# Kernel tuning notes

Measured on AMD Instinct MI355X. Metric: run time of the kernel, lower is better.

## Reference

```python
import jax, jax.numpy as jnp
import numpy as np
from jax import lax

K, INC, OUC = 6, 64, 32
H, W = 512, 512
WIN = 128  # min(128, min(H,W)) for training path
ITERATION = 2  # torch uses random.randint(1,3); fixed for determinism


def setup_inputs() -> dict:
    key = jax.random.key(0)
    ks = jax.random.split(key, 12)
    s = 0.05
    return {
        "x": jax.random.uniform(ks[0], (K, 3, H, W), jnp.float32),
        "pred_list": jax.random.uniform(ks[1], (K, 3, H, W), jnp.float32),
        "feat_list": jax.random.normal(ks[2], (K, INC, H, W), jnp.float32) * 0.1,
        "split_w": jax.random.normal(ks[3], (3 * OUC, INC, 3, 3), jnp.float32) * s,
        "split_b": jax.random.normal(ks[4], (3 * OUC,), jnp.float32) * s,
        "merge1_w": jax.random.normal(ks[5], (INC, 3 * OUC + 3, 3, 3), jnp.float32) * s,
        "merge1_b": jax.random.normal(ks[6], (INC,), jnp.float32) * s,
        "merge2_w": jax.random.normal(ks[7], (INC, INC, 3, 3), jnp.float32) * s,
        "merge2_b": jax.random.normal(ks[8], (INC,), jnp.float32) * s,
        "head_w": jax.random.normal(ks[9], (3, INC, 3, 3), jnp.float32) * s,
        "head_b": jax.random.normal(ks[10], (3,), jnp.float32) * s,
    }


def _conv(x, w, b, groups=1):
    y = lax.conv_general_dilated(
        x, w, (1, 1), ((1, 1), (1, 1)),
        dimension_numbers=("NCHW", "OIHW", "NCHW"), feature_group_count=groups)
    return y + b[None, :, None, None]


def _get_box(pred_list):
    # B_cat = mean of bg channel, T_cat = sum of fg channel; distance map [H,W]
    B_cat = pred_list[:, 2].mean(axis=0)
    T_cat = pred_list[:, 0].sum(axis=0)
    distance = jnp.abs(1.0 - T_cat - B_cat)
    # nearest-neighbor downsample by 0.1: out[i,j] = in[10*i, 10*j]
    hs, ws = H // 10, W // 10
    ds = distance[::10, ::10][:hs, :ws]
    # NMS keep[0] (training path uses boxes[0:1]) == global argmax of score
    idx = jnp.argmax(ds.reshape(-1))
    cx = (idx % ws) * 10
    cy = (idx // ws) * 10
    half = WIN // 2
    x1, y1 = cx - half, cy - half
    x2, y2 = cx + half, cy + half
    ox = (-jnp.minimum(x1, 0) + jnp.minimum(W - x1, 0)
          - jnp.minimum(x2, 0) + jnp.minimum(W - x2, 0))
    oy = (-jnp.minimum(y1, 0) + jnp.minimum(H - y1, 0)
          - jnp.minimum(y2, 0) + jnp.minimum(H - y2, 0))
    return (y1 + oy).astype(jnp.int32), (x1 + ox).astype(jnp.int32)


def reference(x, pred_list, feat_list, split_w, split_b,
              merge1_w, merge1_b, merge2_w, merge2_b, head_w, head_b):
    c = INC
    y1, x1 = _get_box(pred_list)  # box fixed across iterations (computed once)
    x_patch = lax.dynamic_slice(x, (0, 0, y1, x1), (K, 3, WIN, WIN))
    feat_patch = lax.dynamic_slice(feat_list, (0, 0, y1, x1), (K, INC, WIN, WIN))
    feat_tiled = jnp.tile(feat_patch, (1, 3, 1, 1))
    denom = max(K - 1, 1)

    pl = pred_list
    for _ in range(ITERATION):
        pred_patch = lax.dynamic_slice(pl, (0, 0, y1, x1), (K, 3, WIN, WIN))
        # cat([p0.repeat(c), p1.repeat(c), p2.repeat(c)]) == repeat each channel c times
        attention = jnp.repeat(pred_patch, c, axis=1)
        fs = _conv(feat_tiled * attention, split_w, split_b, groups=3)
        f0, f1, f2 = fs[:, :OUC], fs[:, OUC:2 * OUC], fs[:, 2 * OUC:]
        feat_t = f1.sum(0, keepdims=True) / denom - f0.sum(0, keepdims=True) + 2.0 * f0
        feat_r = f0.sum(0, keepdims=True) - f0 + f1
        feat_b = jnp.broadcast_to(f2.mean(0, keepdims=True), f2.shape)
        fcat = jnp.concatenate([feat_t, feat_r, feat_b, x_patch], axis=1)
        h1 = jax.nn.leaky_relu(_conv(fcat, merge1_w, merge1_b), 0.2)
        fm = _conv(h1, merge2_w, merge2_b)
        pr = _conv(fm, head_w, head_b)
        inner = (jnp.tanh(pr[:, :, 10:WIN - 10, 10:WIN - 10]) + 1.0) / 2.0
        pl = lax.dynamic_update_slice(pl, inner, (0, 0, y1 + 10, x1 + 10))
    return pl
```

## Files before the change

### kernel.cpp

```cpp
#include <hip/hip_runtime.h>
#include <math.h>

typedef __attribute__((ext_vector_type(8))) short short8_t;
typedef __attribute__((ext_vector_type(4))) float f32x4;

#define Hh 512
#define Ww 512
#define IMG (Hh * Ww)
#define WINP 128
#define PP (WINP * WINP)
#define QS 325

__device__ __forceinline__ unsigned short f2bf(float f) {
    unsigned int u = __builtin_bit_cast(unsigned int, f);
    u += 0x7fffu + ((u >> 16) & 1u);
    return (unsigned short)(u >> 16);
}
__device__ __forceinline__ float bf2f(unsigned short h) {
    unsigned int u = ((unsigned int)h) << 16;
    return __builtin_bit_cast(float, u);
}

__global__ void box_kernel(const float* __restrict__ pred, int* __restrict__ box) {
    int tid = threadIdx.x;
    float best = -1.0f; int bidx = 0x7fffffff;
    for (int cand = tid; cand < 51 * 51; cand += 256) {
        int i = cand / 51, j = cand % 51;
        int y = i * 10, x = j * 10;
        float T = 0.f, Bv = 0.f;
#pragma unroll
        for (int k = 0; k < 6; ++k) {
            T  += pred[((k * 3 + 0) * Hh + y) * Ww + x];
            Bv += pred[((k * 3 + 2) * Hh + y) * Ww + x];
        }
        float d = fabsf(1.0f - T - Bv / 6.0f);
        if (d > best || (d == best && cand < bidx)) { best = d; bidx = cand; }
    }
    __shared__ float sv[256];
    __shared__ int   si[256];
    sv[tid] = best; si[tid] = bidx;
    __syncthreads();
    for (int s = 128; s > 0; s >>= 1) {
        if (tid < s) {
            if (sv[tid + s] > sv[tid] || (sv[tid + s] == sv[tid] && si[tid + s] < si[tid])) {
                sv[tid] = sv[tid + s]; si[tid] = si[tid + s];
            }
        }
        __syncthreads();
    }
    if (tid == 0) {
        int idx = si[0];
        int cy = (idx / 51) * 10, cx = (idx % 51) * 10;
        int yy = cy - 64; yy = yy < 0 ? 0 : (yy > Hh - WINP ? Hh - WINP : yy);
        int xx = cx - 64; xx = xx < 0 ? 0 : (xx > Ww - WINP ? Ww - WINP : xx);
        box[0] = yy; box[1] = xx;
    }
}

__global__ void copy_kernel(const float4* __restrict__ src, float4* __restrict__ dst) {
    int i = blockIdx.x * 256 + threadIdx.x;
    dst[i] = src[i];
}

__global__ void prep_weights(const float* __restrict__ sw, const float* __restrict__ m1w,
                             const float* __restrict__ m2w, const float* __restrict__ hw,
                             unsigned short* __restrict__ WF)
{
    int idx = blockIdx.x * 256 + threadIdx.x;
    int j = idx & 7;
    int lane = (idx >> 3) & 63;
    int frag = idx >> 9;
    int n16 = lane & 15;
    int ko = (lane >> 4) * 8 + j;
    float v = 0.f;
    if (frag < 108) {
        int g = frag / 36; int r = frag % 36; int kc = r / 18; r %= 18; int tap = r / 2; int nf = r & 1;
        int oc = g * 32 + nf * 16 + n16; int ic = kc * 32 + ko;
        v = sw[(oc * 64 + ic) * 9 + tap];
    } else if (frag < 252) {
        int r = frag - 108; int half = r / 72; r %= 72; int kc = r / 18; r %= 18; int tap = r / 2; int nf = r & 1;
        int oc = half * 32 + nf * 16 + n16; int ic = kc * 32 + ko;
        if (ic < 99) v = m1w[(oc * 99 + ic) * 9 + tap];
    } else if (frag < 324) {
        int r = frag - 252; int half = r / 36; r %= 36; int kc = r / 18; r %= 18; int tap = r / 2; int nf = r & 1;
        int oc = half * 32 + nf * 16 + n16; int ic = kc * 32 + ko;
        v = m2w[(oc * 64 + ic) * 9 + tap];
    } else {
        int r = frag - 324; int kc = r / 9; int tap = r % 9;
        int ic = kc * 32 + ko;
        if (n16 < 3) v = hw[(n16 * 64 + ic) * 9 + tap];
    }
    WF[idx] = f2bf(v);
}

__global__ void prep_featcl(const float* __restrict__ feat, const int* __restrict__ box,
                            unsigned short* __restrict__ featcl)
{
    int row = blockIdx.x;
    int k = blockIdx.y;
    int t = threadIdx.x;
    int y1 = box[0], x1 = box[1];
    __shared__ unsigned short s[128 * 64];
    for (int i = 0; i < 32; ++i) {
        int idx = t + i * 256;
        int ic = idx >> 7, c = idx & 127;
        s[c * 64 + ic] = f2bf(feat[((size_t)(k * 64 + ic) * Hh + y1 + row) * Ww + x1 + c]);
    }
    __syncthreads();
    if (t < 128) {
        unsigned short* dst = &featcl[((size_t)k * 16384 + row * 128 + t) * 64];
        for (int i = 0; i < 8; ++i)
            *(short8_t*)&dst[i * 8] = *(short8_t*)&s[t * 64 + i * 8];
    }
}

__global__ __launch_bounds__(256) void split_mfma(
    const unsigned short* __restrict__ featcl, const float* __restrict__ pl,
    const unsigned short* __restrict__ WF, const float* __restrict__ sb,
    const int* __restrict__ box, unsigned short* __restrict__ fscl)
{
    const int tid = threadIdx.x;
    const int l = tid & 63, w = tid >> 6;
    const int T = blockIdx.x;
    const int k = blockIdx.y / 3, g = blockIdx.y % 3;
    const int ty0 = (T >> 3) * 16, tx0 = (T & 7) * 16;
    const int y1 = box[0], x1 = box[1];

    __shared__ __align__(16) unsigned short s_a[4 * QS * 8];
    __shared__ __align__(16) unsigned short s_b[9216];

    f32x4 acc[4][2];
#pragma unroll
    for (int mf = 0; mf < 4; ++mf)
#pragma unroll
        for (int nf = 0; nf < 2; ++nf) acc[mf][nf] = (f32x4){0.f, 0.f, 0.f, 0.f};

    const float* plg = pl + (size_t)(k * 3 + g) * IMG + (size_t)y1 * Ww + x1;
    const unsigned short* fck = featcl + (size_t)k * 16384 * 64;

    for (int kc = 0; kc < 2; ++kc) {
        __syncthreads();
#pragma unroll
        for (int i = 0; i < 6; ++i) {
            int s = tid + i * 256;
            if (s < 1296) {
                int pxs = s >> 2, q = s & 3;
                int r = pxs / 18, c = pxs - r * 18;
                int py = ty0 - 1 + r, px = tx0 - 1 + c;
                short8_t o;
                if (py >= 0 && py < WINP && px >= 0 && px < WINP) {
                    float pv = plg[py * Ww + px];
                    short8_t f = *(const short8_t*)&fck[(size_t)(py * WINP + px) * 64 + kc * 32 + q * 8];
#pragma unroll
                    for (int e = 0; e < 8; ++e) o[e] = (short)f2bf(bf2f((unsigned short)f[e]) * pv);
                } else {
#pragma unroll
                    for (int e = 0; e < 8; ++e) o[e] = 0;
                }
                *(short8_t*)&s_a[(q * QS + pxs) * 8] = o;
            }
        }
        {
            const unsigned short* src = WF + (size_t)((g * 2 + kc) * 18) * 512;
#pragma unroll
            for (int i = 0; i < 5; ++i) {
                int cch = tid + i * 256;
                if (cch < 1152)
                    *(short8_t*)&s_b[cch * 8] = *(const short8_t*)&src[cch * 8];
            }
        }
        __syncthreads();
#pragma unroll
        for (int tap = 0; tap < 9; ++tap) {
            int dy = tap / 3, dx = tap % 3;
            short8_t a[4];
#pragma unroll
            for (int mf = 0; mf < 4; ++mf)
                a[mf] = *(const short8_t*)&s_a[((l >> 4) * QS + (w * 4 + mf + dy) * 18 + (l & 15) + dx) * 8];
#pragma unroll
            for (int nf = 0; nf < 2; ++nf) {
                short8_t bfr = *(const short8_t*)&s_b[((tap * 2 + nf) * 64 + l) * 8];
#pragma unroll
                for (int mf = 0; mf < 4; ++mf)
                    acc[mf][nf] = __builtin_amdgcn_mfma_f32_16x16x32_bf16(a[mf], bfr, acc[mf][nf], 0, 0, 0);
            }
        }
    }
    __syncthreads();
    unsigned short* s_t = s_a;
#pragma unroll
    for (int nf = 0; nf < 2; ++nf) {
        float bias = sb[g * 32 + nf * 16 + (l & 15)];
        int slot = nf * 2 + ((l & 15) >> 3);
#pragma unroll
        for (int mf = 0; mf < 4; ++mf) {
            int row = w * 4 + mf;
#pragma unroll
            for (int r = 0; r < 4; ++r) {
                int col = (l >> 4) * 4 + r;
                s_t[(slot * 256 + row * 16 + col) * 8 + (l & 7)] = f2bf(acc[mf][nf][r] + bias);
            }
        }
    }
    __syncthreads();
    {
        int row = tid >> 4, col = tid & 15;
        size_t gpx = (size_t)(ty0 + row) * WINP + tx0 + col;
        unsigned short* dst = fscl + ((size_t)k * 16384 + gpx) * 96 + g * 32;
#pragma unroll
        for (int i = 0; i < 4; ++i)
            *(short8_t*)&dst[i * 8] = *(short8_t*)&s_t[(i * 256 + tid) * 8];
    }
}

__global__ void reduce_kernel(const unsigned short* __restrict__ fscl, float* __restrict__ Scl)
{
    int tg = blockIdx.x * 256 + threadIdx.x;
    int px = tg >> 2, q = tg & 3;
    float s0[8], s1[8], s2[8];
#pragma unroll
    for (int e = 0; e < 8; ++e) { s0[e] = 0.f; s1[e] = 0.f; s2[e] = 0.f; }
#pragma unroll
    for (int k = 0; k < 6; ++k) {
        const unsigned short* p = &fscl[((size_t)k * 16384 + px) * 96 + q * 8];
        short8_t a0 = *(const short8_t*)&p[0];
        short8_t a1 = *(const short8_t*)&p[32];
        short8_t a2 = *(const short8_t*)&p[64];
#pragma unroll
        for (int e = 0; e < 8; ++e) {
            s0[e] += bf2f((unsigned short)a0[e]);
            s1[e] += bf2f((unsigned short)a1[e]);
            s2[e] += bf2f((unsigned short)a2[e]);
        }
    }
    float* d = &Scl[(size_t)px * 96 + q * 8];
#pragma unroll
    for (int e = 0; e < 8; ++e) {
        d[e]      = s1[e] * 0.2f - s0[e];
        d[32 + e] = s0[e];
        d[64 + e] = s2[e] * (1.f / 6.f);
    }
}

__global__ __launch_bounds__(256) void merge1_mfma(
    const unsigned short* __restrict__ fscl, const float* __restrict__ Scl,
    const float* __restrict__ x, const unsigned short* __restrict__ WF,
    const float* __restrict__ m1b, const int* __restrict__ box,
    unsigned short* __restrict__ h1cl)
{
    const int tid = threadIdx.x;
    const int l = tid & 63, w = tid >> 6;
    const int T = blockIdx.x;
    const int k = blockIdx.y >> 1, half = blockIdx.y & 1;
    const int ty0 = (T >> 3) * 16, tx0 = (T & 7) * 16;
    const int y1 = box[0], x1 = box[1];

    __shared__ __align__(16) unsigned short s_a[4 * QS * 8];
    __shared__ __align__(16) unsigned short s_b[9216];

    f32x4 acc[4][2];
#pragma unroll
    for (int mf = 0; mf < 4; ++mf)
#pragma unroll
        for (int nf = 0; nf < 2; ++nf) acc[mf][nf] = (f32x4){0.f, 0.f, 0.f, 0.f};

    for (int kc = 0; kc < 4; ++kc) {
        __syncthreads();
#pragma unroll
        for (int i = 0; i < 6; ++i) {
            int s = tid + i * 256;
            if (s < 1296) {
                int pxs = s >> 2, q = s & 3;
                int r = pxs / 18, c = pxs - r * 18;
                int py = ty0 - 1 + r, px = tx0 - 1 + c;
                short8_t o;
#pragma unroll
                for (int e = 0; e < 8; ++e) o[e] = 0;
                if (py >= 0 && py < WINP && px >= 0 && px < WINP) {
                    size_t gpx = (size_t)py * WINP + px;
                    if (kc == 0) {
                        short8_t f0 = *(const short8_t*)&fscl[((size_t)k * 16384 + gpx) * 96 + q * 8];
                        const float* S = &Scl[gpx * 96 + q * 8];
#pragma unroll
                        for (int e = 0; e < 8; ++e)
                            o[e] = (short)f2bf(S[e] + 2.f * bf2f((unsigned short)f0[e]));
                    } else if (kc == 1) {
                        const unsigned short* fp = &fscl[((size_t)k * 16384 + gpx) * 96];
                        short8_t f0 = *(const short8_t*)&fp[q * 8];
                        short8_t f1 = *(const short8_t*)&fp[32 + q * 8];
                        const float* S = &Scl[gpx * 96 + 32 + q * 8];
#pragma unroll
                        for (int e = 0; e < 8; ++e)
                            o[e] = (short)f2bf(S[e] - bf2f((unsigned short)f0[e]) + bf2f((unsigned short)f1[e]));
                    } else if (kc == 2) {
                        const float* S = &Scl[gpx * 96 + 64 + q * 8];
#pragma unroll
                        for (int e = 0; e < 8; ++e) o[e] = (short)f2bf(S[e]);
                    } else {
                        if (q == 0) {
#pragma unroll
                            for (int ch = 0; ch < 3; ++ch)
                                o[ch] = (short)f2bf(x[(size_t)(k * 3 + ch) * IMG + (size_t)(y1 + py) * Ww + x1 + px]);
                        }
                    }
                }
                *(short8_t*)&s_a[(q * QS + pxs) * 8] = o;
            }
        }
        {
            const unsigned short* src = WF + (size_t)(108 + (half * 4 + kc) * 18) * 512;
#pragma unroll
            for (int i = 0; i < 5; ++i) {
                int cch = tid + i * 256;
                if (cch < 1152)
                    *(short8_t*)&s_b[cch * 8] = *(const short8_t*)&src[cch * 8];
            }
        }
        __syncthreads();
#pragma unroll
        for (int tap = 0; tap < 9; ++tap) {
            int dy = tap / 3, dx = tap % 3;
            short8_t a[4];
#pragma unroll
            for (int mf = 0; mf < 4; ++mf)
                a[mf] = *(const short8_t*)&s_a[((l >> 4) * QS + (w * 4 + mf + dy) * 18 + (l & 15) + dx) * 8];
#pragma unroll
            for (int nf = 0; nf < 2; ++nf) {
                short8_t bfr = *(const short8_t*)&s_b[((tap * 2 + nf) * 64 + l) * 8];
#pragma unroll
                for (int mf = 0; mf < 4; ++mf)
                    acc[mf][nf] = __builtin_amdgcn_mfma_f32_16x16x32_bf16(a[mf], bfr, acc[mf][nf], 0, 0, 0);
            }
        }
    }
    __syncthreads();
    unsigned short* s_t = s_a;
#pragma unroll
    for (int nf = 0; nf < 2; ++nf) {
        float bias = m1b[half * 32 + nf * 16 + (l & 15)];
        int slot = nf * 2 + ((l & 15) >> 3);
#pragma unroll
        for (int mf = 0; mf < 4; ++mf) {
            int row = w * 4 + mf;
#pragma unroll
            for (int r = 0; r < 4; ++r) {
                int col = (l >> 4) * 4 + r;
                float v = acc[mf][nf][r] + bias;
                v = v >= 0.f ? v : 0.2f * v;
                s_t[(slot * 256 + row * 16 + col) * 8 + (l & 7)] = f2bf(v);
            }
        }
    }
    __syncthreads();
    {
        int row = tid >> 4, col = tid & 15;
        size_t gpx = (size_t)(ty0 + row) * WINP + tx0 + col;
        unsigned short* dst = h1cl + ((size_t)k * 16384 + gpx) * 64 + half * 32;
#pragma unroll
        for (int i = 0; i < 4; ++i)
            *(short8_t*)&dst[i * 8] = *(short8_t*)&s_t[(i * 256 + tid) * 8];
    }
}

__global__ __launch_bounds__(256) void merge2_mfma(
    const unsigned short* __restrict__ h1cl, const unsigned short* __restrict__ WF,
    const float* __restrict__ m2b, unsigned short* __restrict__ h2cl)
{
    const int tid = threadIdx.x;
    const int l = tid & 63, w = tid >> 6;
    const int T = blockIdx.x;
    const int k = blockIdx.y >> 1, half = blockIdx.y & 1;
    const int ty0 = (T >> 3) * 16, tx0 = (T & 7) * 16;

    __shared__ __align__(16) unsigned short s_a[4 * QS * 8];
    __shared__ __align__(16) unsigned short s_b[9216];

    f32x4 acc[4][2];
#pragma unroll
    for (int mf = 0; mf < 4; ++mf)
#pragma unroll
        for (int nf = 0; nf < 2; ++nf) acc[mf][nf] = (f32x4){0.f, 0.f, 0.f, 0.f};

    const unsigned short* ink = h1cl + (size_t)k * 16384 * 64;

    for (int kc = 0; kc < 2; ++kc) {
        __syncthreads();
#pragma unroll
        for (int i = 0; i < 6; ++i) {
            int s = tid + i * 256;
            if (s < 1296) {
                int pxs = s >> 2, q = s & 3;
                int r = pxs / 18, c = pxs - r * 18;
                int py = ty0 - 1 + r, px = tx0 - 1 + c;
                short8_t o;
                if (py >= 0 && py < WINP && px >= 0 && px < WINP) {
                    o = *(const short8_t*)&ink[(size_t)(py * WINP + px) * 64 + kc * 32 + q * 8];
                } else {
#pragma unroll
                    for (int e = 0; e < 8; ++e) o[e] = 0;
                }
                *(short8_t*)&s_a[(q * QS + pxs) * 8] = o;
            }
        }
        {
            const unsigned short* src = WF + (size_t)(252 + (half * 2 + kc) * 18) * 512;
#pragma unroll
            for (int i = 0; i < 5; ++i) {
                int cch = tid + i * 256;
                if (cch < 1152)
                    *(short8_t*)&s_b[cch * 8] = *(const short8_t*)&src[cch * 8];
            }
        }
        __syncthreads();
#pragma unroll
        for (int tap = 0; tap < 9; ++tap) {
            int dy = tap / 3, dx = tap % 3;
            short8_t a[4];
#pragma unroll
            for (int mf = 0; mf < 4; ++mf)
                a[mf] = *(const short8_t*)&s_a[((l >> 4) * QS + (w * 4 + mf + dy) * 18 + (l & 15) + dx) * 8];
#pragma unroll
            for (int nf = 0; nf < 2; ++nf) {
                short8_t bfr = *(const short8_t*)&s_b[((tap * 2 + nf) * 64 + l) * 8];
#pragma unroll
                for (int mf = 0; mf < 4; ++mf)
                    acc[mf][nf] = __builtin_amdgcn_mfma_f32_16x16x32_bf16(a[mf], bfr, acc[mf][nf], 0, 0, 0);
            }
        }
    }
    __syncthreads();
    unsigned short* s_t = s_a;
#pragma unroll
    for (int nf = 0; nf < 2; ++nf) {
        float bias = m2b[half * 32 + nf * 16 + (l & 15)];
        int slot = nf * 2 + ((l & 15) >> 3);
#pragma unroll
        for (int mf = 0; mf < 4; ++mf) {
            int row = w * 4 + mf;
#pragma unroll
            for (int r = 0; r < 4; ++r) {
                int col = (l >> 4) * 4 + r;
                s_t[(slot * 256 + row * 16 + col) * 8 + (l & 7)] = f2bf(acc[mf][nf][r] + bias);
            }
        }
    }
    __syncthreads();
    {
        int row = tid >> 4, col = tid & 15;
        size_t gpx = (size_t)(ty0 + row) * WINP + tx0 + col;
        unsigned short* dst = h2cl + ((size_t)k * 16384 + gpx) * 64 + half * 32;
#pragma unroll
        for (int i = 0; i < 4; ++i)
            *(short8_t*)&dst[i * 8] = *(short8_t*)&s_t[(i * 256 + tid) * 8];
    }
}

__global__ __launch_bounds__(256) void head_mfma(
    const unsigned short* __restrict__ h2cl, const unsigned short* __restrict__ WF,
    const float* __restrict__ hb, const int* __restrict__ box,
    float* __restrict__ out)
{
    const int tid = threadIdx.x;
    const int l = tid & 63, w = tid >> 6;
    const int T = blockIdx.x;
    const int k = blockIdx.y;
    const int oy0 = 10 + (T / 7) * 16, ox0 = 10 + (T % 7) * 16;
    const int y1 = box[0], x1 = box[1];

    __shared__ __align__(16) unsigned short s_a[4 * QS * 8];
    __shared__ __align__(16) unsigned short s_b[4608];

    f32x4 acc[4];
#pragma unroll
    for (int mf = 0; mf < 4; ++mf) acc[mf] = (f32x4){0.f, 0.f, 0.f, 0.f};

    const unsigned short* ink = h2cl + (size_t)k * 16384 * 64;

    for (int kc = 0; kc < 2; ++kc) {
        __syncthreads();
#pragma unroll
        for (int i = 0; i < 6; ++i) {
            int s = tid + i * 256;
            if (s < 1296) {
                int pxs = s >> 2, q = s & 3;
                int r = pxs / 18, c = pxs - r * 18;
                int py = oy0 - 1 + r, px = ox0 - 1 + c;
                *(short8_t*)&s_a[(q * QS + pxs) * 8] =
                    *(const short8_t*)&ink[(size_t)(py * WINP + px) * 64 + kc * 32 + q * 8];
            }
        }
        {
            const unsigned short* src = WF + (size_t)(324 + kc * 9) * 512;
#pragma unroll
            for (int i = 0; i < 3; ++i) {
                int cch = tid + i * 256;
                if (cch < 576)
                    *(short8_t*)&s_b[cch * 8] = *(const short8_t*)&src[cch * 8];
            }
        }
        __syncthreads();
#pragma unroll
        for (int tap = 0; tap < 9; ++tap) {
            int dy = tap / 3, dx = tap % 3;
            short8_t bfr = *(const short8_t*)&s_b[(tap * 64 + l) * 8];
#pragma unroll
            for (int mf = 0; mf < 4; ++mf) {
                short8_t a = *(const short8_t*)&s_a[((l >> 4) * QS + (w * 4 + mf + dy) * 18 + (l & 15) + dx) * 8];
                acc[mf] = __builtin_amdgcn_mfma_f32_16x16x32_bf16(a, bfr, acc[mf], 0, 0, 0);
            }
        }
    }
    int oc = l & 15;
    if (oc < 3) {
        float bias = hb[oc];
#pragma unroll
        for (int mf = 0; mf < 4; ++mf) {
            int row = oy0 + w * 4 + mf;
            if (row < 118) {
#pragma unroll
                for (int r = 0; r < 4; ++r) {
                    int col = ox0 + (l >> 4) * 4 + r;
                    if (col < 118) {
                        float v = (tanhf(acc[mf][r] + bias) + 1.0f) * 0.5f;
                        out[(size_t)(k * 3 + oc) * IMG + (size_t)(y1 + row) * Ww + x1 + col] = v;
                    }
                }
            }
        }
    }
}

extern "C" void kernel_launch(void* const* d_in, const int* in_sizes, int n_in,
                              void* d_out, int out_size, void* d_ws, size_t ws_size,
                              hipStream_t stream)
{
    const float* x       = (const float*)d_in[0];
    const float* pred    = (const float*)d_in[1];
    const float* feat    = (const float*)d_in[2];
    const float* split_w = (const float*)d_in[3];
    const float* split_b = (const float*)d_in[4];
    const float* m1w     = (const float*)d_in[5];
    const float* m1b     = (const float*)d_in[6];
    const float* m2w     = (const float*)d_in[7];
    const float* m2b     = (const float*)d_in[8];
    const float* hw      = (const float*)d_in[9];
    const float* hb      = (const float*)d_in[10];
    float* out = (float*)d_out;

    char* base = (char*)d_ws;
    size_t o = 0;
    int* box = (int*)(base + o);                  o += 256;
    unsigned short* WF = (unsigned short*)(base + o);      o += (size_t)175104 * 2;  o = (o + 255) & ~(size_t)255;
    unsigned short* featcl = (unsigned short*)(base + o);  o += (size_t)6 * 16384 * 64 * 2;
    unsigned short* fscl = (unsigned short*)(base + o);    o += (size_t)6 * 16384 * 96 * 2;
    float* Scl = (float*)(base + o);                       o += (size_t)16384 * 96 * 4;
    unsigned short* h1cl = (unsigned short*)(base + o);    o += (size_t)6 * 16384 * 64 * 2;
    unsigned short* h2cl = (unsigned short*)(base + o);    o += (size_t)6 * 16384 * 64 * 2;

    box_kernel<<<1, 256, 0, stream>>>(pred, box);
    prep_weights<<<684, 256, 0, stream>>>(split_w, m1w, m2w, hw, WF);
    prep_featcl<<<dim3(128, 6), 256, 0, stream>>>(feat, box, featcl);
    copy_kernel<<<4608, 256, 0, stream>>>((const float4*)pred, (float4*)out);

    for (int it = 0; it < 2; ++it) {
        split_mfma<<<dim3(64, 18), 256, 0, stream>>>(featcl, out, WF, split_b, box, fscl);
        reduce_kernel<<<256, 256, 0, stream>>>(fscl, Scl);
        merge1_mfma<<<dim3(64, 12), 256, 0, stream>>>(fscl, Scl, x, WF, m1b, box, h1cl);
        merge2_mfma<<<dim3(64, 12), 256, 0, stream>>>(h1cl, WF, m2b, h2cl);
        head_mfma<<<dim3(49, 6), 256, 0, stream>>>(h2cl, WF, hb, box, out);
    }
}
```

Measured before the change: 694.5 us.

## Split MFMA conv work by output-channel half per wave and merge prologue kernels

Each wave in the split, merge1 and merge2 conv kernels now owns one 16-channel output fragment over 8 rows, instead of both fragments over 4 rows. It keeps all 9 weight taps in registers and walks the input rows once, reusing each loaded A row across the three dy taps. This cuts LDS reads per MFMA, at the cost of more registers for the accumulators and cached weights. The head kernel gets the same row-reuse loop, and the box, weight-prep and copy kernels are fused into one launch to remove launch overhead.

```diff
diff --git a/kernel.cpp b/kernel.cpp
--- a/kernel.cpp
+++ b/kernel.cpp
@@ -21,12 +21,51 @@
     return __builtin_bit_cast(float, u);
 }
 
-__global__ void box_kernel(const float* __restrict__ pred, int* __restrict__ box) {
+__global__ void prologue_kernel(const float* __restrict__ pred, int* __restrict__ box,
+                                const float* __restrict__ sw, const float* __restrict__ m1w,
+                                const float* __restrict__ m2w, const float* __restrict__ hw,
+                                unsigned short* __restrict__ WF,
+                                const float4* __restrict__ csrc, float4* __restrict__ cdst)
+{
+    int b = blockIdx.x;
     int tid = threadIdx.x;
+    if (b < 684) {
+        int idx = b * 256 + tid;
+        int j = idx & 7;
+        int lane = (idx >> 3) & 63;
+        int frag = idx >> 9;
+        int n16 = lane & 15;
+        int ko = (lane >> 4) * 8 + j;
+        float v = 0.f;
+        if (frag < 108) {
+            int g = frag / 36; int r = frag % 36; int kc = r / 18; r %= 18; int tap = r / 2; int nf = r & 1;
+            int oc = g * 32 + nf * 16 + n16; int ic = kc * 32 + ko;
+            v = sw[(oc * 64 + ic) * 9 + tap];
+        } else if (frag < 252) {
+            int r = frag - 108; int half = r / 72; r %= 72; int kc = r / 18; r %= 18; int tap = r / 2; int nf = r & 1;
+            int oc = half * 32 + nf * 16 + n16; int ic = kc * 32 + ko;
+            if (ic < 99) v = m1w[(oc * 99 + ic) * 9 + tap];
+        } else if (frag < 324) {
+            int r = frag - 252; int half = r / 36; r %= 36; int kc = r / 18; r %= 18; int tap = r / 2; int nf = r & 1;
+            int oc = half * 32 + nf * 16 + n16; int ic = kc * 32 + ko;
+            v = m2w[(oc * 64 + ic) * 9 + tap];
+        } else {
+            int r = frag - 324; int kc = r / 9; int tap = r % 9;
+            int ic = kc * 32 + ko;
+            if (n16 < 3) v = hw[(n16 * 64 + ic) * 9 + tap];
+        }
+        WF[idx] = f2bf(v);
+        return;
+    }
+    if (b < 5292) {
+        int i = (b - 684) * 256 + tid;
+        cdst[i] = csrc[i];
+        return;
+    }
     float best = -1.0f; int bidx = 0x7fffffff;
     for (int cand = tid; cand < 51 * 51; cand += 256) {
-        int i = cand / 51, j = cand % 51;
-        int y = i * 10, x = j * 10;
+        int i = cand / 51, jj = cand % 51;
+        int y = i * 10, x = jj * 10;
         float T = 0.f, Bv = 0.f;
 #pragma unroll
         for (int k = 0; k < 6; ++k) {
@@ -55,42 +94,6 @@
         int xx = cx - 64; xx = xx < 0 ? 0 : (xx > Ww - WINP ? Ww - WINP : xx);
         box[0] = yy; box[1] = xx;
     }
-}
-
-__global__ void copy_kernel(const float4* __restrict__ src, float4* __restrict__ dst) {
-    int i = blockIdx.x * 256 + threadIdx.x;
-    dst[i] = src[i];
-}
-
-__global__ void prep_weights(const float* __restrict__ sw, const float* __restrict__ m1w,
-                             const float* __restrict__ m2w, const float* __restrict__ hw,
-                             unsigned short* __restrict__ WF)
-{
-    int idx = blockIdx.x * 256 + threadIdx.x;
-    int j = idx & 7;
-    int lane = (idx >> 3) & 63;
-    int frag = idx >> 9;
-    int n16 = lane & 15;
-    int ko = (lane >> 4) * 8 + j;
-    float v = 0.f;
-    if (frag < 108) {
-        int g = frag / 36; int r = frag % 36; int kc = r / 18; r %= 18; int tap = r / 2; int nf = r & 1;
-        int oc = g * 32 + nf * 16 + n16; int ic = kc * 32 + ko;
-        v = sw[(oc * 64 + ic) * 9 + tap];
-    } else if (frag < 252) {
-        int r = frag - 108; int half = r / 72; r %= 72; int kc = r / 18; r %= 18; int tap = r / 2; int nf = r & 1;
-        int oc = half * 32 + nf * 16 + n16; int ic = kc * 32 + ko;
-        if (ic < 99) v = m1w[(oc * 99 + ic) * 9 + tap];
-    } else if (frag < 324) {
-        int r = frag - 252; int half = r / 36; r %= 36; int kc = r / 18; r %= 18; int tap = r / 2; int nf = r & 1;
-        int oc = half * 32 + nf * 16 + n16; int ic = kc * 32 + ko;
-        v = m2w[(oc * 64 + ic) * 9 + tap];
-    } else {
-        int r = frag - 324; int kc = r / 9; int tap = r % 9;
-        int ic = kc * 32 + ko;
-        if (n16 < 3) v = hw[(n16 * 64 + ic) * 9 + tap];
-    }
-    WF[idx] = f2bf(v);
 }
 
 __global__ void prep_featcl(const float* __restrict__ feat, const int* __restrict__ box,
@@ -114,6 +117,7 @@
     }
 }
 
+
 __global__ __launch_bounds__(256) void split_mfma(
     const unsigned short* __restrict__ featcl, const float* __restrict__ pl,
     const unsigned short* __restrict__ WF, const float* __restrict__ sb,
@@ -125,15 +129,15 @@
     const int k = blockIdx.y / 3, g = blockIdx.y % 3;
     const int ty0 = (T >> 3) * 16, tx0 = (T & 7) * 16;
     const int y1 = box[0], x1 = box[1];
+    const int nf = w & 1;
+    const int rbase = (w >> 1) * 8;
 
     __shared__ __align__(16) unsigned short s_a[4 * QS * 8];
     __shared__ __align__(16) unsigned short s_b[9216];
 
-    f32x4 acc[4][2];
-#pragma unroll
-    for (int mf = 0; mf < 4; ++mf)
-#pragma unroll
-        for (int nf = 0; nf < 2; ++nf) acc[mf][nf] = (f32x4){0.f, 0.f, 0.f, 0.f};
+    f32x4 acc[8];
+#pragma unroll
+    for (int mf = 0; mf < 8; ++mf) acc[mf] = (f32x4){0.f, 0.f, 0.f, 0.f};
 
     const float* plg = pl + (size_t)(k * 3 + g) * IMG + (size_t)y1 * Ww + x1;
     const unsigned short* fck = featcl + (size_t)k * 16384 * 64;
@@ -170,35 +174,39 @@
             }
         }
         __syncthreads();
-#pragma unroll
-        for (int tap = 0; tap < 9; ++tap) {
-            int dy = tap / 3, dx = tap % 3;
-            short8_t a[4];
-#pragma unroll
-            for (int mf = 0; mf < 4; ++mf)
-                a[mf] = *(const short8_t*)&s_a[((l >> 4) * QS + (w * 4 + mf + dy) * 18 + (l & 15) + dx) * 8];
-#pragma unroll
-            for (int nf = 0; nf < 2; ++nf) {
-                short8_t bfr = *(const short8_t*)&s_b[((tap * 2 + nf) * 64 + l) * 8];
-#pragma unroll
-                for (int mf = 0; mf < 4; ++mf)
-                    acc[mf][nf] = __builtin_amdgcn_mfma_f32_16x16x32_bf16(a[mf], bfr, acc[mf][nf], 0, 0, 0);
+        short8_t breg[9];
+#pragma unroll
+        for (int tap = 0; tap < 9; ++tap)
+            breg[tap] = *(const short8_t*)&s_b[((tap * 2 + nf) * 64 + l) * 8];
+#pragma unroll
+        for (int r = 0; r < 10; ++r) {
+            short8_t av[3];
+#pragma unroll
+            for (int dx = 0; dx < 3; ++dx)
+                av[dx] = *(const short8_t*)&s_a[((l >> 4) * QS + (rbase + r) * 18 + (l & 15) + dx) * 8];
+#pragma unroll
+            for (int dy = 0; dy < 3; ++dy) {
+                const int mf = r - dy;
+                if (mf >= 0 && mf < 8) {
+#pragma unroll
+                    for (int dx = 0; dx < 3; ++dx)
+                        acc[mf] = __builtin_amdgcn_mfma_f32_16x16x32_bf16(av[dx], breg[dy * 3 + dx], acc[mf], 0, 0, 0);
+                }
             }
         }
     }
     __syncthreads();
     unsigned short* s_t = s_a;
-#pragma unroll
-    for (int nf = 0; nf < 2; ++nf) {
+    {
         float bias = sb[g * 32 + nf * 16 + (l & 15)];
         int slot = nf * 2 + ((l & 15) >> 3);
 #pragma unroll
-        for (int mf = 0; mf < 4; ++mf) {
-            int row = w * 4 + mf;
+        for (int mf = 0; mf < 8; ++mf) {
+            int row = rbase + mf;
 #pragma unroll
             for (int r = 0; r < 4; ++r) {
                 int col = (l >> 4) * 4 + r;
-                s_t[(slot * 256 + row * 16 + col) * 8 + (l & 7)] = f2bf(acc[mf][nf][r] + bias);
+                s_t[(slot * 256 + row * 16 + col) * 8 + (l & 7)] = f2bf(acc[mf][r] + bias);
             }
         }
     }
@@ -254,15 +262,15 @@
     const int k = blockIdx.y >> 1, half = blockIdx.y & 1;
     const int ty0 = (T >> 3) * 16, tx0 = (T & 7) * 16;
     const int y1 = box[0], x1 = box[1];
+    const int nf = w & 1;
+    const int rbase = (w >> 1) * 8;
 
     __shared__ __align__(16) unsigned short s_a[4 * QS * 8];
     __shared__ __align__(16) unsigned short s_b[9216];
 
-    f32x4 acc[4][2];
-#pragma unroll
-    for (int mf = 0; mf < 4; ++mf)
-#pragma unroll
-        for (int nf = 0; nf < 2; ++nf) acc[mf][nf] = (f32x4){0.f, 0.f, 0.f, 0.f};
+    f32x4 acc[8];
+#pragma unroll
+    for (int mf = 0; mf < 8; ++mf) acc[mf] = (f32x4){0.f, 0.f, 0.f, 0.f};
 
     for (int kc = 0; kc < 4; ++kc) {
         __syncthreads();
@@ -317,35 +325,39 @@
             }
         }
         __syncthreads();
-#pragma unroll
-        for (int tap = 0; tap < 9; ++tap) {
-            int dy = tap / 3, dx = tap % 3;
-            short8_t a[4];
-#pragma unroll
-            for (int mf = 0; mf < 4; ++mf)
-                a[mf] = *(const short8_t*)&s_a[((l >> 4) * QS + (w * 4 + mf + dy) * 18 + (l & 15) + dx) * 8];
-#pragma unroll
-            for (int nf = 0; nf < 2; ++nf) {
-                short8_t bfr = *(const short8_t*)&s_b[((tap * 2 + nf) * 64 + l) * 8];
-#pragma unroll
-                for (int mf = 0; mf < 4; ++mf)
-                    acc[mf][nf] = __builtin_amdgcn_mfma_f32_16x16x32_bf16(a[mf], bfr, acc[mf][nf], 0, 0, 0);
+        short8_t breg[9];
+#pragma unroll
+        for (int tap = 0; tap < 9; ++tap)
+            breg[tap] = *(const short8_t*)&s_b[((tap * 2 + nf) * 64 + l) * 8];
+#pragma unroll
+        for (int r = 0; r < 10; ++r) {
+            short8_t av[3];
+#pragma unroll
+            for (int dx = 0; dx < 3; ++dx)
+                av[dx] = *(const short8_t*)&s_a[((l >> 4) * QS + (rbase + r) * 18 + (l & 15) + dx) * 8];
+#pragma unroll
+            for (int dy = 0; dy < 3; ++dy) {
+                const int mf = r - dy;
+                if (mf >= 0 && mf < 8) {
+#pragma unroll
+                    for (int dx = 0; dx < 3; ++dx)
+                        acc[mf] = __builtin_amdgcn_mfma_f32_16x16x32_bf16(av[dx], breg[dy * 3 + dx], acc[mf], 0, 0, 0);
+                }
             }
         }
     }
     __syncthreads();
     unsigned short* s_t = s_a;
-#pragma unroll
-    for (int nf = 0; nf < 2; ++nf) {
+    {
         float bias = m1b[half * 32 + nf * 16 + (l & 15)];
         int slot = nf * 2 + ((l & 15) >> 3);
 #pragma unroll
-        for (int mf = 0; mf < 4; ++mf) {
-            int row = w * 4 + mf;
+        for (int mf = 0; mf < 8; ++mf) {
+            int row = rbase + mf;
 #pragma unroll
             for (int r = 0; r < 4; ++r) {
                 int col = (l >> 4) * 4 + r;
-                float v = acc[mf][nf][r] + bias;
+                float v = acc[mf][r] + bias;
                 v = v >= 0.f ? v : 0.2f * v;
                 s_t[(slot * 256 + row * 16 + col) * 8 + (l & 7)] = f2bf(v);
             }
@@ -371,15 +383,15 @@
     const int T = blockIdx.x;
     const int k = blockIdx.y >> 1, half = blockIdx.y & 1;
     const int ty0 = (T >> 3) * 16, tx0 = (T & 7) * 16;
+    const int nf = w & 1;
+    const int rbase = (w >> 1) * 8;
 
     __shared__ __align__(16) unsigned short s_a[4 * QS * 8];
     __shared__ __align__(16) unsigned short s_b[9216];
 
-    f32x4 acc[4][2];
-#pragma unroll
-    for (int mf = 0; mf < 4; ++mf)
-#pragma unroll
-        for (int nf = 0; nf < 2; ++nf) acc[mf][nf] = (f32x4){0.f, 0.f, 0.f, 0.f};
+    f32x4 acc[8];
+#pragma unroll
+    for (int mf = 0; mf < 8; ++mf) acc[mf] = (f32x4){0.f, 0.f, 0.f, 0.f};
 
     const unsigned short* ink = h1cl + (size_t)k * 16384 * 64;
 
@@ -412,35 +424,39 @@
             }
         }
         __syncthreads();
-#pragma unroll
-        for (int tap = 0; tap < 9; ++tap) {
-            int dy = tap / 3, dx = tap % 3;
-            short8_t a[4];
-#pragma unroll
-            for (int mf = 0; mf < 4; ++mf)
-                a[mf] = *(const short8_t*)&s_a[((l >> 4) * QS + (w * 4 + mf + dy) * 18 + (l & 15) + dx) * 8];
-#pragma unroll
-            for (int nf = 0; nf < 2; ++nf) {
-                short8_t bfr = *(const short8_t*)&s_b[((tap * 2 + nf) * 64 + l) * 8];
-#pragma unroll
-                for (int mf = 0; mf < 4; ++mf)
-                    acc[mf][nf] = __builtin_amdgcn_mfma_f32_16x16x32_bf16(a[mf], bfr, acc[mf][nf], 0, 0, 0);
+        short8_t breg[9];
+#pragma unroll
+        for (int tap = 0; tap < 9; ++tap)
+            breg[tap] = *(const short8_t*)&s_b[((tap * 2 + nf) * 64 + l) * 8];
+#pragma unroll
+        for (int r = 0; r < 10; ++r) {
+            short8_t av[3];
+#pragma unroll
+            for (int dx = 0; dx < 3; ++dx)
+                av[dx] = *(const short8_t*)&s_a[((l >> 4) * QS + (rbase + r) * 18 + (l & 15) + dx) * 8];
+#pragma unroll
+            for (int dy = 0; dy < 3; ++dy) {
+                const int mf = r - dy;
+                if (mf >= 0 && mf < 8) {
+#pragma unroll
+                    for (int dx = 0; dx < 3; ++dx)
+                        acc[mf] = __builtin_amdgcn_mfma_f32_16x16x32_bf16(av[dx], breg[dy * 3 + dx], acc[mf], 0, 0, 0);
+                }
             }
         }
     }
     __syncthreads();
     unsigned short* s_t = s_a;
-#pragma unroll
-    for (int nf = 0; nf < 2; ++nf) {
+    {
         float bias = m2b[half * 32 + nf * 16 + (l & 15)];
         int slot = nf * 2 + ((l & 15) >> 3);
 #pragma unroll
-        for (int mf = 0; mf < 4; ++mf) {
-            int row = w * 4 + mf;
+        for (int mf = 0; mf < 8; ++mf) {
+            int row = rbase + mf;
 #pragma unroll
             for (int r = 0; r < 4; ++r) {
                 int col = (l >> 4) * 4 + r;
-                s_t[(slot * 256 + row * 16 + col) * 8 + (l & 7)] = f2bf(acc[mf][nf][r] + bias);
+                s_t[(slot * 256 + row * 16 + col) * 8 + (l & 7)] = f2bf(acc[mf][r] + bias);
             }
         }
     }
@@ -499,14 +515,24 @@
             }
         }
         __syncthreads();
-#pragma unroll
-        for (int tap = 0; tap < 9; ++tap) {
-            int dy = tap / 3, dx = tap % 3;
-            short8_t bfr = *(const short8_t*)&s_b[(tap * 64 + l) * 8];
-#pragma unroll
-            for (int mf = 0; mf < 4; ++mf) {
-                short8_t a = *(const short8_t*)&s_a[((l >> 4) * QS + (w * 4 + mf + dy) * 18 + (l & 15) + dx) * 8];
-                acc[mf] = __builtin_amdgcn_mfma_f32_16x16x32_bf16(a, bfr, acc[mf], 0, 0, 0);
+        short8_t breg[9];
+#pragma unroll
+        for (int tap = 0; tap < 9; ++tap)
+            breg[tap] = *(const short8_t*)&s_b[(tap * 64 + l) * 8];
+#pragma unroll
+        for (int r = 0; r < 6; ++r) {
+            short8_t av[3];
+#pragma unroll
+            for (int dx = 0; dx < 3; ++dx)
+                av[dx] = *(const short8_t*)&s_a[((l >> 4) * QS + (w * 4 + r) * 18 + (l & 15) + dx) * 8];
+#pragma unroll
+            for (int dy = 0; dy < 3; ++dy) {
+                const int mf = r - dy;
+                if (mf >= 0 && mf < 4) {
+#pragma unroll
+                    for (int dx = 0; dx < 3; ++dx)
+                        acc[mf] = __builtin_amdgcn_mfma_f32_16x16x32_bf16(av[dx], breg[dy * 3 + dx], acc[mf], 0, 0, 0);
+                }
             }
         }
     }
@@ -557,10 +583,9 @@
     unsigned short* h1cl = (unsigned short*)(base + o);    o += (size_t)6 * 16384 * 64 * 2;
     unsigned short* h2cl = (unsigned short*)(base + o);    o += (size_t)6 * 16384 * 64 * 2;
 
-    box_kernel<<<1, 256, 0, stream>>>(pred, box);
-    prep_weights<<<684, 256, 0, stream>>>(split_w, m1w, m2w, hw, WF);
+    prologue_kernel<<<5293, 256, 0, stream>>>(pred, box, split_w, m1w, m2w, hw, WF,
+                                              (const float4*)pred, (float4*)out);
     prep_featcl<<<dim3(128, 6), 256, 0, stream>>>(feat, box, featcl);
-    copy_kernel<<<4608, 256, 0, stream>>>((const float4*)pred, (float4*)out);
 
     for (int it = 0; it < 2; ++it) {
         split_mfma<<<dim3(64, 18), 256, 0, stream>>>(featcl, out, WF, split_b, box, fscl);
```

Result: faster. 658.3 us (-5.2%).
